# Performance work log

Hardware: AMD Instinct MI355X
Metric: run time of the kernel (lower is better)

The kernel has to match this reference:

```python
import jax, jax.numpy as jnp
import numpy as np

NUM_HEADS_SPLIT = 12   # hardcoded in einops reduce pattern
NUM_HEADS_SCALE = 8    # num_heads used only for scale computation (module bug, kept faithful)


def setup_inputs() -> dict:
    key = jax.random.key(0)
    ks = jax.random.split(key, 5)
    B, P, D = 32, 577, 768
    return {
        "x": jax.random.normal(ks[0], (B, P, D), dtype=jnp.float32),
        "qkv_w": jax.random.normal(ks[1], (3 * D, D), dtype=jnp.float32) * 0.02,
        "qkv_b": jax.random.normal(ks[2], (3 * D,), dtype=jnp.float32) * 0.02,
        "out_w": jax.random.normal(ks[3], (D, D), dtype=jnp.float32) * 0.02,
        "out_b": jax.random.normal(ks[4], (D,), dtype=jnp.float32) * 0.02,
    }


def reference(x, qkv_w, qkv_b, out_w, out_b):
    B, P, D = x.shape
    h = NUM_HEADS_SPLIT
    s = D // h
    scale = (D // NUM_HEADS_SCALE) ** -0.5  # 96**-0.5, per original code

    # qkv projection: [B, P, 3D]
    qkv = jnp.einsum('bpd,ed->bpe', x, qkv_w) + qkv_b
    # reshape 'b p (c h s) -> b p c h s' (reduce with mean is a pure reshape here)
    qkv = qkv.reshape(B, P, 3, h, s)
    # split order in the original: v, q, k
    v = jnp.transpose(qkv[:, :, 0], (0, 2, 1, 3))  # [B, h, P, s]
    q = jnp.transpose(qkv[:, :, 1], (0, 2, 1, 3))
    k = jnp.transpose(qkv[:, :, 2], (0, 2, 1, 3))

    attn = jnp.einsum('bhps,bhqs->bhpq', q, k) * scale
    attn = jax.nn.softmax(attn, axis=-1)
    out = jnp.einsum('bhpq,bhqs->bhps', attn, v)  # [B, h, P, s]
    out = jnp.transpose(out, (0, 2, 1, 3)).reshape(B, P, D)

    return jnp.einsum('bpd,ed->bpe', out, out_w) + out_b
```

## Files before the change

kernel.cpp:

```cpp
#include <hip/hip_runtime.h>
#include <stdint.h>

typedef __attribute__((ext_vector_type(8))) short short8;
typedef __attribute__((ext_vector_type(4))) float floatx4;

#define DEV static __device__ __forceinline__

constexpr int Bb = 32, Pp = 577, Dd = 768, Hh = 12;
constexpr int M_VALID = Bb * Pp;
constexpr int M_PAD   = 18560;
constexpr int PKV     = 640;
constexpr float SCALE = 0.10206207261596577f;

DEV ushort f2b(float f) {
  union { float f; uint32_t u; } c; c.f = f;
  uint32_t u = c.u + 0x7fffu + ((c.u >> 16) & 1u);
  return (ushort)(u >> 16);
}

__global__ void cvt_pad(const float* __restrict__ src, ushort* __restrict__ dst,
                        int n_valid4, int n_total4) {
  const float4* s4 = (const float4*)src;
  for (int i = blockIdx.x * blockDim.x + threadIdx.x; i < n_total4;
       i += gridDim.x * blockDim.x) {
    float4 v = make_float4(0.f, 0.f, 0.f, 0.f);
    if (i < n_valid4) v = s4[i];
    ushort4 o;
    o.x = f2b(v.x); o.y = f2b(v.y); o.z = f2b(v.z); o.w = f2b(v.w);
    ((ushort4*)dst)[i] = o;
  }
}

template<bool C_F32>
__global__ __launch_bounds__(256) void gemm_bt(
    const ushort* __restrict__ A, int lda,
    const ushort* __restrict__ Bw,
    const float* __restrict__ bias, void* __restrict__ Cout,
    int N, int K, int m_valid)
{
  __shared__ ushort As[128 * 32];
  __shared__ ushort Bs[128 * 32];
  const int tid = threadIdx.x;
  const int lane = tid & 63;
  const int w = tid >> 6;
  const int wr = w >> 1, wc = w & 1;
  const int llo = lane & 15, lhi = lane >> 4;
  const int m0 = blockIdx.x * 128, n0 = blockIdx.y * 128;

  floatx4 acc[4][4];
#pragma unroll
  for (int i = 0; i < 4; ++i)
#pragma unroll
    for (int j = 0; j < 4; ++j) acc[i][j] = floatx4{0.f, 0.f, 0.f, 0.f};

  const int srow = tid >> 2;
  const int scol = (tid & 3) * 8;
  const ushort* gA0 = A  + (size_t)(m0 + srow) * lda + scol;
  const ushort* gA1 = A  + (size_t)(m0 + 64 + srow) * lda + scol;
  const ushort* gB0 = Bw + (size_t)(n0 + srow) * K + scol;
  const ushort* gB1 = Bw + (size_t)(n0 + 64 + srow) * K + scol;
  ushort* lA0 = As + tid * 8;
  ushort* lA1 = As + 2048 + tid * 8;
  ushort* lB0 = Bs + tid * 8;
  ushort* lB1 = Bs + 2048 + tid * 8;

  for (int kk = 0; kk < K; kk += 32) {
    __builtin_amdgcn_global_load_lds(
        (const __attribute__((address_space(1))) void*)(gA0 + kk),
        (__attribute__((address_space(3))) void*)lA0, 16, 0, 0);
    __builtin_amdgcn_global_load_lds(
        (const __attribute__((address_space(1))) void*)(gA1 + kk),
        (__attribute__((address_space(3))) void*)lA1, 16, 0, 0);
    __builtin_amdgcn_global_load_lds(
        (const __attribute__((address_space(1))) void*)(gB0 + kk),
        (__attribute__((address_space(3))) void*)lB0, 16, 0, 0);
    __builtin_amdgcn_global_load_lds(
        (const __attribute__((address_space(1))) void*)(gB1 + kk),
        (__attribute__((address_space(3))) void*)lB1, 16, 0, 0);
    __syncthreads();

    short8 af[4], bfr[4];
#pragma unroll
    for (int i = 0; i < 4; ++i) {
      af[i]  = *(const short8*)(As + (wr * 64 + i * 16 + llo) * 32 + lhi * 8);
      bfr[i] = *(const short8*)(Bs + (wc * 64 + i * 16 + llo) * 32 + lhi * 8);
    }
#pragma unroll
    for (int i = 0; i < 4; ++i)
#pragma unroll
      for (int j = 0; j < 4; ++j)
        acc[i][j] = __builtin_amdgcn_mfma_f32_16x16x32_bf16(af[i], bfr[j], acc[i][j], 0, 0, 0);
    __syncthreads();
  }

  float bv[4];
#pragma unroll
  for (int j = 0; j < 4; ++j) bv[j] = bias[n0 + wc * 64 + j * 16 + llo];

#pragma unroll
  for (int i = 0; i < 4; ++i) {
#pragma unroll
    for (int r = 0; r < 4; ++r) {
      const int row = m0 + wr * 64 + i * 16 + lhi * 4 + r;
      if (C_F32 && row >= m_valid) continue;
      const size_t rb = (size_t)row * N + n0 + wc * 64;
#pragma unroll
      for (int j = 0; j < 4; ++j) {
        float v = acc[i][j][r] + bv[j];
        if (C_F32) ((float*)Cout)[rb + j * 16 + llo] = v;
        else       ((ushort*)Cout)[rb + j * 16 + llo] = f2b(v);
      }
    }
  }
}

__global__ __launch_bounds__(256) void vtrans(const ushort* __restrict__ C1,
                                              ushort* __restrict__ Vt) {
  const int pt = blockIdx.x, h = blockIdx.y, b = blockIdx.z;
  __shared__ ushort Ts[64][72];
  const int t = threadIdx.x;
  const int rl = t >> 2, c16 = (t & 3) * 16;
  const int p = pt * 64 + rl;
  short8 a0 = {0,0,0,0,0,0,0,0}, a1 = {0,0,0,0,0,0,0,0};
  if (p < Pp) {
    const ushort* s = C1 + (size_t)(b * Pp + p) * 2304 + h * 64 + c16;
    a0 = *(const short8*)s;
    a1 = *(const short8*)(s + 8);
  }
  *(short8*)&Ts[rl][c16] = a0;
  *(short8*)&Ts[rl][c16 + 8] = a1;
  __syncthreads();
  const int ss = t >> 2, pc16 = (t & 3) * 16;
  short8 o0, o1;
#pragma unroll
  for (int i = 0; i < 8; ++i) {
    o0[i] = (short)Ts[pc16 + i][ss];
    o1[i] = (short)Ts[pc16 + 8 + i][ss];
  }
  ushort* d = Vt + ((size_t)(b * Hh + h) * 64 + ss) * PKV + pt * 64 + pc16;
  *(short8*)d = o0;
  *(short8*)(d + 8) = o1;
}

__global__ __launch_bounds__(256) void attn_fwd(
    ushort* C1, const ushort* __restrict__ Vt)
{
  const int qt = blockIdx.x, h = blockIdx.y, b = blockIdx.z;
  const int tid = threadIdx.x;
  const int lane = tid & 63, w = tid >> 6;
  const int llo = lane & 15, lhi = lane >> 4;

  __shared__ ushort Ks[64][72];
  __shared__ ushort Vs[64][72];
  __shared__ ushort Ps[4][16][72];

  const int q0 = qt * 64;
  const int qrow = q0 + w * 16 + llo;
  const size_t qoff = (size_t)(b * Pp + qrow) * 2304 + 768 + h * 64;
  const short8 qf0 = *(const short8*)(C1 + qoff + lhi * 8);
  const short8 qf1 = *(const short8*)(C1 + qoff + 32 + lhi * 8);

  float ls[4] = {0.f, 0.f, 0.f, 0.f};
  floatx4 acc_o[4];
#pragma unroll
  for (int st = 0; st < 4; ++st) acc_o[st] = floatx4{0.f, 0.f, 0.f, 0.f};

  const int srow = tid >> 2;
  const int sc16 = (tid & 3) * 16;
  const ushort* kbase = C1 + (size_t)(b * Pp + srow) * 2304 + 1536 + h * 64 + sc16;
  const ushort* vbase = Vt + ((size_t)(b * Hh + h) * 64 + srow) * PKV + sc16;

  for (int t = 0; t < 10; ++t) {
    const short8 k0 = *(const short8*)(kbase + (size_t)t * 64 * 2304);
    const short8 k1 = *(const short8*)(kbase + (size_t)t * 64 * 2304 + 8);
    const short8 v0 = *(const short8*)(vbase + t * 64);
    const short8 v1 = *(const short8*)(vbase + t * 64 + 8);
    __syncthreads();
    *(short8*)&Ks[srow][sc16] = k0;
    *(short8*)&Ks[srow][sc16 + 8] = k1;
    *(short8*)&Vs[srow][sc16] = v0;
    *(short8*)&Vs[srow][sc16 + 8] = v1;
    __syncthreads();

    float pv[4][4];
#pragma unroll
    for (int ntl = 0; ntl < 4; ++ntl) {
      floatx4 acc = floatx4{0.f, 0.f, 0.f, 0.f};
      const short8 bf0 = *(const short8*)&Ks[ntl * 16 + llo][lhi * 8];
      const short8 bf1 = *(const short8*)&Ks[ntl * 16 + llo][32 + lhi * 8];
      acc = __builtin_amdgcn_mfma_f32_16x16x32_bf16(qf0, bf0, acc, 0, 0, 0);
      acc = __builtin_amdgcn_mfma_f32_16x16x32_bf16(qf1, bf1, acc, 0, 0, 0);
      const bool valid = (t * 64 + ntl * 16 + llo) < Pp;
#pragma unroll
      for (int r = 0; r < 4; ++r) {
        const float p = valid ? __expf(acc[r] * SCALE) : 0.f;
        pv[ntl][r] = p;
        ls[r] += p;
      }
    }

#pragma unroll
    for (int r = 0; r < 4; ++r)
#pragma unroll
      for (int ntl = 0; ntl < 4; ++ntl)
        Ps[w][lhi * 4 + r][ntl * 16 + llo] = f2b(pv[ntl][r]);

    const short8 pa0 = *(const short8*)&Ps[w][llo][lhi * 8];
    const short8 pa1 = *(const short8*)&Ps[w][llo][32 + lhi * 8];
#pragma unroll
    for (int st = 0; st < 4; ++st) {
      const short8 vb0 = *(const short8*)&Vs[st * 16 + llo][lhi * 8];
      const short8 vb1 = *(const short8*)&Vs[st * 16 + llo][32 + lhi * 8];
      acc_o[st] = __builtin_amdgcn_mfma_f32_16x16x32_bf16(pa0, vb0, acc_o[st], 0, 0, 0);
      acc_o[st] = __builtin_amdgcn_mfma_f32_16x16x32_bf16(pa1, vb1, acc_o[st], 0, 0, 0);
    }
  }

#pragma unroll
  for (int r = 0; r < 4; ++r) {
#pragma unroll
    for (int off = 1; off < 16; off <<= 1) ls[r] += __shfl_xor(ls[r], off, 64);
  }

#pragma unroll
  for (int r = 0; r < 4; ++r) {
    const int p = q0 + w * 16 + lhi * 4 + r;
    if (p < Pp) {
      const float inv = 1.f / ls[r];
      const size_t ob = (size_t)(b * Pp + p) * 2304 + h * 64;
#pragma unroll
      for (int st = 0; st < 4; ++st)
        C1[ob + st * 16 + llo] = f2b(acc_o[st][r] * inv);
    }
  }
}

extern "C" void kernel_launch(void* const* d_in, const int* in_sizes, int n_in,
                              void* d_out, int out_size, void* d_ws, size_t ws_size,
                              hipStream_t stream) {
  const float* x     = (const float*)d_in[0];
  const float* qkv_w = (const float*)d_in[1];
  const float* qkv_b = (const float*)d_in[2];
  const float* out_w = (const float*)d_in[3];
  const float* out_b = (const float*)d_in[4];
  float* out = (float*)d_out;

  char* ws = (char*)d_ws;
  ushort* C1b = (ushort*)(ws);
  ushort* W3b = (ushort*)(ws + 85524480);
  ushort* W1b = (ushort*)(ws + 86704128);
  ushort* Xb  = (ushort*)(ws + 90243072);
  ushort* Vtb = (ushort*)(ws + 86704128);

  cvt_pad<<<2048, 256, 0, stream>>>(x, Xb, M_VALID * 768 / 4, M_PAD * 768 / 4);
  cvt_pad<<<1024, 256, 0, stream>>>(qkv_w, W1b, 2304 * 768 / 4, 2304 * 768 / 4);
  cvt_pad<<<512, 256, 0, stream>>>(out_w, W3b, 768 * 768 / 4, 768 * 768 / 4);

  gemm_bt<false><<<dim3(145, 18), 256, 0, stream>>>(Xb, 768, W1b, qkv_b,
                                                    (void*)C1b, 2304, 768, M_PAD);
  vtrans<<<dim3(10, 12, 32), 256, 0, stream>>>(C1b, Vtb);
  attn_fwd<<<dim3(10, 12, 32), 256, 0, stream>>>(C1b, Vtb);
  gemm_bt<true><<<dim3(145, 6), 256, 0, stream>>>(C1b, 2304, W3b, out_b,
                                                  (void*)out, 768, 768, M_VALID);
}
```

Before: 384.5 us.

## Double-buffer GEMM LDS tiles and remap workgroups per XCD

The bf16 GEMM kernel now uses two LDS buffers and issues the next k-tile's global-to-LDS loads before computing on the current one, with explicit vmcnt waits and barriers, so load latency overlaps MFMA work. The launch changes to a 1D grid, and the block index is remapped so consecutive tiles land on the same XCD, which is meant to improve L2 reuse of A/B tiles. LDS use doubles, which may reduce occupancy. The hand-written waitcnt counts depend on the compiler's load ordering.

```diff
diff --git a/kernel.cpp b/kernel.cpp
--- a/kernel.cpp
+++ b/kernel.cpp
@@ -31,21 +31,49 @@
   }
 }
 
+#define STAGE(bi, kk)                                                          \
+  do {                                                                         \
+    __builtin_amdgcn_global_load_lds(                                          \
+        (const __attribute__((address_space(1))) void*)(gA0 + (kk)),           \
+        (__attribute__((address_space(3))) void*)(As + (bi)*4096 + tid * 8),   \
+        16, 0, 0);                                                             \
+    __builtin_amdgcn_global_load_lds(                                          \
+        (const __attribute__((address_space(1))) void*)(gA1 + (kk)),           \
+        (__attribute__((address_space(3))) void*)(As + (bi)*4096 + 2048 + tid * 8), \
+        16, 0, 0);                                                             \
+    __builtin_amdgcn_global_load_lds(                                          \
+        (const __attribute__((address_space(1))) void*)(gB0 + (kk)),           \
+        (__attribute__((address_space(3))) void*)(Bs + (bi)*4096 + tid * 8),   \
+        16, 0, 0);                                                             \
+    __builtin_amdgcn_global_load_lds(                                          \
+        (const __attribute__((address_space(1))) void*)(gB1 + (kk)),           \
+        (__attribute__((address_space(3))) void*)(Bs + (bi)*4096 + 2048 + tid * 8), \
+        16, 0, 0);                                                             \
+  } while (0)
+
 template<bool C_F32>
 __global__ __launch_bounds__(256) void gemm_bt(
     const ushort* __restrict__ A, int lda,
     const ushort* __restrict__ Bw,
     const float* __restrict__ bias, void* __restrict__ Cout,
-    int N, int K, int m_valid)
+    int N, int K, int m_valid, int nt_n)
 {
-  __shared__ ushort As[128 * 32];
-  __shared__ ushort Bs[128 * 32];
+  __shared__ ushort As[2 * 128 * 32];
+  __shared__ ushort Bs[2 * 128 * 32];
   const int tid = threadIdx.x;
   const int lane = tid & 63;
   const int w = tid >> 6;
   const int wr = w >> 1, wc = w & 1;
   const int llo = lane & 15, lhi = lane >> 4;
-  const int m0 = blockIdx.x * 128, n0 = blockIdx.y * 128;
+
+  {
+  }
+  const int nwg = gridDim.x;
+  const int L = blockIdx.x;
+  const int q = nwg >> 3, r = nwg & 7;
+  const int xcd = L & 7, pos = L >> 3;
+  const int wgid = (xcd < r ? xcd * (q + 1) : r * (q + 1) + (xcd - r) * q) + pos;
+  const int m0 = (wgid / nt_n) * 128, n0 = (wgid % nt_n) * 128;
 
   floatx4 acc[4][4];
 #pragma unroll
@@ -59,38 +87,36 @@
   const ushort* gA1 = A  + (size_t)(m0 + 64 + srow) * lda + scol;
   const ushort* gB0 = Bw + (size_t)(n0 + srow) * K + scol;
   const ushort* gB1 = Bw + (size_t)(n0 + 64 + srow) * K + scol;
-  ushort* lA0 = As + tid * 8;
-  ushort* lA1 = As + 2048 + tid * 8;
-  ushort* lB0 = Bs + tid * 8;
-  ushort* lB1 = Bs + 2048 + tid * 8;
-
+
+  STAGE(0, 0);
+  int cur = 0;
   for (int kk = 0; kk < K; kk += 32) {
-    __builtin_amdgcn_global_load_lds(
-        (const __attribute__((address_space(1))) void*)(gA0 + kk),
-        (__attribute__((address_space(3))) void*)lA0, 16, 0, 0);
-    __builtin_amdgcn_global_load_lds(
-        (const __attribute__((address_space(1))) void*)(gA1 + kk),
-        (__attribute__((address_space(3))) void*)lA1, 16, 0, 0);
-    __builtin_amdgcn_global_load_lds(
-        (const __attribute__((address_space(1))) void*)(gB0 + kk),
-        (__attribute__((address_space(3))) void*)lB0, 16, 0, 0);
-    __builtin_amdgcn_global_load_lds(
-        (const __attribute__((address_space(1))) void*)(gB1 + kk),
-        (__attribute__((address_space(3))) void*)lB1, 16, 0, 0);
-    __syncthreads();
-
+    if (kk + 32 < K) {
+      STAGE(cur ^ 1, kk + 32);
+      asm volatile("s_waitcnt vmcnt(4)" ::: "memory");
+    } else {
+      asm volatile("s_waitcnt vmcnt(0)" ::: "memory");
+    }
+    __builtin_amdgcn_s_barrier();
+    __builtin_amdgcn_sched_barrier(0);
+
+    const ushort* Ab = As + cur * 4096;
+    const ushort* Bb = Bs + cur * 4096;
     short8 af[4], bfr[4];
 #pragma unroll
     for (int i = 0; i < 4; ++i) {
-      af[i]  = *(const short8*)(As + (wr * 64 + i * 16 + llo) * 32 + lhi * 8);
-      bfr[i] = *(const short8*)(Bs + (wc * 64 + i * 16 + llo) * 32 + lhi * 8);
+      af[i]  = *(const short8*)(Ab + (wr * 64 + i * 16 + llo) * 32 + lhi * 8);
+      bfr[i] = *(const short8*)(Bb + (wc * 64 + i * 16 + llo) * 32 + lhi * 8);
     }
 #pragma unroll
     for (int i = 0; i < 4; ++i)
 #pragma unroll
       for (int j = 0; j < 4; ++j)
         acc[i][j] = __builtin_amdgcn_mfma_f32_16x16x32_bf16(af[i], bfr[j], acc[i][j], 0, 0, 0);
-    __syncthreads();
+
+    __builtin_amdgcn_sched_barrier(0);
+    __builtin_amdgcn_s_barrier();
+    cur ^= 1;
   }
 
   float bv[4];
@@ -100,13 +126,13 @@
 #pragma unroll
   for (int i = 0; i < 4; ++i) {
 #pragma unroll
-    for (int r = 0; r < 4; ++r) {
-      const int row = m0 + wr * 64 + i * 16 + lhi * 4 + r;
+    for (int r2 = 0; r2 < 4; ++r2) {
+      const int row = m0 + wr * 64 + i * 16 + lhi * 4 + r2;
       if (C_F32 && row >= m_valid) continue;
       const size_t rb = (size_t)row * N + n0 + wc * 64;
 #pragma unroll
       for (int j = 0; j < 4; ++j) {
-        float v = acc[i][j][r] + bv[j];
+        float v = acc[i][j][r2] + bv[j];
         if (C_F32) ((float*)Cout)[rb + j * 16 + llo] = v;
         else       ((ushort*)Cout)[rb + j * 16 + llo] = f2b(v);
       }
@@ -256,10 +282,10 @@
   cvt_pad<<<1024, 256, 0, stream>>>(qkv_w, W1b, 2304 * 768 / 4, 2304 * 768 / 4);
   cvt_pad<<<512, 256, 0, stream>>>(out_w, W3b, 768 * 768 / 4, 768 * 768 / 4);
 
-  gemm_bt<false><<<dim3(145, 18), 256, 0, stream>>>(Xb, 768, W1b, qkv_b,
-                                                    (void*)C1b, 2304, 768, M_PAD);
+  gemm_bt<false><<<dim3(145 * 18), 256, 0, stream>>>(Xb, 768, W1b, qkv_b,
+                                                     (void*)C1b, 2304, 768, M_PAD, 18);
   vtrans<<<dim3(10, 12, 32), 256, 0, stream>>>(C1b, Vtb);
   attn_fwd<<<dim3(10, 12, 32), 256, 0, stream>>>(C1b, Vtb);
-  gemm_bt<true><<<dim3(145, 6), 256, 0, stream>>>(C1b, 2304, W3b, out_b,
-                                                  (void*)out, 768, 768, M_VALID);
-}
+  gemm_bt<true><<<dim3(145 * 6), 256, 0, stream>>>(C1b, 2304, W3b, out_b,
+                                                   (void*)out, 768, 768, M_VALID, 6);
+}
```

Result: faster. 350.9 us (-8.7%).
